# Kernel tuning notes

Measured on AMD Instinct MI355X. Metric: run time of the kernel, lower is better.

The kernel has to match this reference:

```python
import math
import jax, jax.numpy as jnp
import numpy as np

B, A, M, NC = 32, 8400, 32, 80
TOP_K, ALPHA, BETA, EPS = 13, 1.0, 6.0, 1e-9
IMG = 640.0


def _ciou(b1, b2, eps=1e-7):
    # b1, b2 broadcastable [..., 4]; CIoU as in compute_iou (box1=gt, box2=pred)
    b1x1, b1y1, b1x2, b1y2 = b1[..., 0], b1[..., 1], b1[..., 2], b1[..., 3]
    b2x1, b2y1, b2x2, b2y2 = b2[..., 0], b2[..., 1], b2[..., 2], b2[..., 3]
    w1, h1 = b1x2 - b1x1, b1y2 - b1y1 + eps
    w2, h2 = b2x2 - b2x1, b2y2 - b2y1 + eps
    inter = (jnp.minimum(b1x2, b2x2) - jnp.maximum(b1x1, b2x1)).clip(0) * \
            (jnp.minimum(b1y2, b2y2) - jnp.maximum(b1y1, b2y1)).clip(0)
    union = w1 * h1 + w2 * h2 - inter + eps
    iou = inter / union
    cw = jnp.maximum(b1x2, b2x2) - jnp.minimum(b1x1, b2x1)
    ch = jnp.maximum(b1y2, b2y2) - jnp.minimum(b1y1, b2y1)
    c2 = cw ** 2 + ch ** 2 + eps
    rho2 = ((b2x1 + b2x2 - b1x1 - b1x2) ** 2 + (b2y1 + b2y2 - b1y1 - b1y2) ** 2) / 4.0
    v = (4.0 / math.pi ** 2) * (jnp.arctan(w2 / h2) - jnp.arctan(w1 / h1)) ** 2
    alpha = jax.lax.stop_gradient(v / (v - iou + (1.0 + eps)))
    return iou - (rho2 / c2 + v * alpha)


def setup_inputs() -> dict:
    key = jax.random.key(0)
    ks = jax.random.split(key, 8)
    pd_scores = jax.random.uniform(ks[0], (B, A, NC), jnp.float32)
    anc_points = jax.random.uniform(ks[1], (A, 2), jnp.float32) * IMG
    # predicted boxes around anchor points (valid x1<x2, y1<y2)
    off = jax.random.uniform(ks[2], (B, A, 4), jnp.float32) * 80.0 + 2.0
    pd_bboxes = jnp.concatenate([anc_points[None] - off[..., :2],
                                 anc_points[None] + off[..., 2:]], -1)
    # GT boxes: random centers and sizes, clipped to image
    c = jax.random.uniform(ks[3], (B, M, 2), jnp.float32) * IMG
    wh = jax.random.uniform(ks[4], (B, M, 2), jnp.float32) * 180.0 + 20.0
    gt_bboxes = jnp.concatenate([(c - wh / 2).clip(0, IMG), (c + wh / 2).clip(0, IMG)], -1)
    gt_labels = jax.random.randint(ks[5], (B, M, 1), 0, NC, jnp.int64)
    n_valid = jax.random.randint(ks[6], (B,), 1, M + 1)
    mask_gt = (jnp.arange(M)[None, :] < n_valid[:, None]).astype(jnp.float32)[..., None]
    return {"pd_scores": pd_scores, "pd_bboxes": pd_bboxes, "anc_points": anc_points,
            "gt_labels": gt_labels, "gt_bboxes": gt_bboxes, "mask_gt": mask_gt}


def reference(pd_scores, pd_bboxes, anc_points, gt_labels, gt_bboxes, mask_gt):
    b, a, nc = pd_scores.shape
    m = gt_bboxes.shape[1]
    dtype = pd_scores.dtype

    # anchors-inside-GT mask: [B,M,A]
    lt = gt_bboxes[:, :, None, :2]          # [B,M,1,2]
    rb = gt_bboxes[:, :, None, 2:]
    deltas = jnp.concatenate([anc_points[None, None] - lt,
                              rb - anc_points[None, None]], -1)  # [B,M,A,4]
    mask_in_gts = deltas.min(-1) > EPS
    mg = mask_gt[..., 0] > 0                 # [B,M] bool
    gt_mask = mask_in_gts & mg[:, :, None]

    # per-GT class score gather: pd_scores[b, :, gt_labels[b,m]] -> [B,M,A]
    labels = gt_labels[..., 0]               # [B,M]
    idx = jnp.broadcast_to(labels[:, :, None, None], (b, m, a, 1))
    gathered = jnp.take_along_axis(jnp.broadcast_to(pd_scores[:, None], (b, m, a, nc)), idx, axis=3)[..., 0]
    bbox_scores = jnp.where(gt_mask, gathered, 0.0)

    # CIoU overlaps (dense, masked) [B,M,A]
    iou = _ciou(gt_bboxes[:, :, None, :], pd_bboxes[:, None, :, :])
    overlaps = jnp.where(gt_mask, jnp.maximum(iou, 0.0), 0.0)

    align_metric = bbox_scores ** ALPHA * overlaps ** BETA

    # top-k selection with duplicate suppression (faithful to scatter_add loop)
    _, tk_idx = jax.lax.top_k(align_metric, TOP_K)      # [B,M,K]
    tk_mask = jnp.broadcast_to(mg[:, :, None], tk_idx.shape)
    tk_idx = jnp.where(tk_mask, tk_idx, 0)
    bi = jnp.arange(b)[:, None, None]
    mi = jnp.arange(m)[None, :, None]
    counts = jnp.zeros((b, m, a), jnp.int32).at[bi, mi, tk_idx].add(1)
    mask_top_k = jnp.where(counts > 1, 0, counts).astype(dtype)

    mask_pos = mask_top_k * mask_in_gts.astype(dtype) * mg[:, :, None].astype(dtype)
    fg_mask = mask_pos.sum(1)                            # [B,A]

    # resolve anchors assigned to multiple GTs (no-op when none; matches torch branch)
    mask_multi = fg_mask[:, None, :] > 1                 # [B,M,A] (broadcast)
    max_idx = overlaps.argmax(1)                         # [B,A]
    is_max = (jnp.arange(m)[None, :, None] == max_idx[:, None, :]).astype(dtype)
    mask_pos = jnp.where(mask_multi, is_max, mask_pos)
    fg_mask = mask_pos.sum(1)

    target_gt_idx = mask_pos.argmax(1)                   # [B,A]
    target_labels = jnp.maximum(jnp.take_along_axis(labels, target_gt_idx, axis=1), 0)
    target_bboxes = jnp.take_along_axis(
        gt_bboxes, jnp.broadcast_to(target_gt_idx[..., None], (b, a, 4)), axis=1)

    target_scores = jax.nn.one_hot(target_labels, NC, dtype=dtype)
    target_scores = jnp.where((fg_mask > 0)[..., None], target_scores, 0.0)

    am = align_metric * mask_pos
    pos_am = am.max(-1, keepdims=True)                   # [B,M,1]
    pos_ov = (overlaps * mask_pos).max(-1, keepdims=True)
    norm = (am * pos_ov / (pos_am + EPS)).max(1)[..., None]  # [B,A,1]
    target_scores = target_scores * norm

    return target_bboxes, target_scores, fg_mask > 0
```

## Files before the change

### kernel.cpp

```cpp
#include <hip/hip_runtime.h>
#include <math.h>

#define BB 32
#define AA 8400
#define MM 32
#define NCC 80
#define TOPK 13
#define CAP 1024
#define NW (AA / 32 + 1)

__device__ __forceinline__ void wave_argmax(float& v, int& i) {
    #pragma unroll
    for (int off = 32; off > 0; off >>= 1) {
        float ov = __shfl_xor(v, off, 64);
        int oi = __shfl_xor(i, off, 64);
        if (ov > v || (ov == v && oi < i)) { v = ov; i = oi; }
    }
}

__global__ __launch_bounds__(256) void k0_zero(unsigned int* __restrict__ selmask) {
    int g = blockIdx.x * 256 + threadIdx.x;
    if (g < BB * AA / 4) reinterpret_cast<uint4*>(selmask)[g] = uint4{0u, 0u, 0u, 0u};
}

__global__ __launch_bounds__(256) void k12_topk(
        const float* __restrict__ pd_scores, const float* __restrict__ pd_bboxes,
        const float* __restrict__ anc, const int* __restrict__ gt_labels,
        const float* __restrict__ gt_bboxes, const float* __restrict__ mask_gt,
        unsigned int* __restrict__ selmask, float* __restrict__ pos_am, float* __restrict__ pos_ov) {
    __shared__ float lval[CAP];
    __shared__ int   lidx[CAP];
    __shared__ unsigned int bmask[NW];
    __shared__ float wv[4];
    __shared__ int   wi[4];
    __shared__ int   wsum[4];
    __shared__ int   s_p;
    const float eps = 1e-7f;
    int bm = blockIdx.x;
    int b = bm >> 5;
    int m = bm & 31;
    unsigned int mbit = 1u << m;
    int tid = threadIdx.x;
    int lane = tid & 63;
    int wid = tid >> 6;
    if (tid == 0) pos_am[bm] = 0.f;
    if (tid == 1) pos_ov[bm] = 0.f;
    if (!(mask_gt[bm] > 0.f)) return;
    if (tid == 2) s_p = 0;

    for (int i = tid; i < NW; i += 256) bmask[i] = 0u;
    float4 g = reinterpret_cast<const float4*>(gt_bboxes)[bm];

    const float4* anc4 = reinterpret_cast<const float4*>(anc);
    unsigned long long bits = 0ull;
    int c_t = 0;
    #pragma unroll
    for (int j = 0; j < 17; j++) {
        int e = tid + (j << 8);
        if (e < 4200) {
            float4 an = anc4[e];
            float d0 = fminf(fminf(an.x - g.x, an.y - g.y), fminf(g.z - an.x, g.w - an.y));
            float d1 = fminf(fminf(an.z - g.x, an.w - g.y), fminf(g.z - an.z, g.w - an.w));
            if (d0 > 1e-9f) { bits |= 1ull << (2 * j);     c_t++; }
            if (d1 > 1e-9f) { bits |= 1ull << (2 * j + 1); c_t++; }
        }
    }
    int x = c_t;
    #pragma unroll
    for (int off = 1; off < 64; off <<= 1) {
        int y = __shfl_up(x, off, 64);
        if (lane >= off) x += y;
    }
    if (lane == 63) wsum[wid] = x;
    __syncthreads();
    int base = 0;
    #pragma unroll
    for (int w = 0; w < 4; w++) if (w < wid) base += wsum[w];
    int n_c = min(wsum[0] + wsum[1] + wsum[2] + wsum[3], CAP);
    {
        int o = base + x - c_t;
        unsigned long long mm_ = bits;
        while (mm_) {
            int k = __builtin_ctzll(mm_);
            mm_ &= mm_ - 1ull;
            int i = 2 * tid + 512 * (k >> 1) + (k & 1);
            if (o < CAP) lidx[o] = i;
            o++;
        }
    }
    for (int s = n_c + tid; s < CAP; s += 256) { lval[s] = -1.f; lidx[s] = AA; }
    __syncthreads();

    float w1 = g.z - g.x, h1 = g.w - g.y + eps;
    float atg = atanf(w1 / h1);
    float w1h1 = w1 * h1;
    float sgx = g.x + g.z, sgy = g.y + g.w;
    int lab = gt_labels[bm];
    const float4* pbb = reinterpret_cast<const float4*>(pd_bboxes) + (long)b * AA;
    const float* scp = pd_scores + (long)b * AA * NCC + lab;
    int nit = (n_c + 255) >> 8;
    for (int it = 0; it < nit; it++) {
        int s = (it << 8) + tid;
        bool pos = false;
        if (s < n_c) {
            int i = lidx[s];
            float4 pb = pbb[i];
            float w2 = pb.z - pb.x, h2 = pb.w - pb.y + eps;
            float iw = fmaxf(fminf(g.z, pb.z) - fmaxf(g.x, pb.x), 0.f);
            float ih = fmaxf(fminf(g.w, pb.w) - fmaxf(g.y, pb.y), 0.f);
            float inter = iw * ih;
            float uni = w1h1 + w2 * h2 - inter + eps;
            float iou = inter / uni;
            float cw = fmaxf(g.z, pb.z) - fminf(g.x, pb.x);
            float ch = fmaxf(g.w, pb.w) - fminf(g.y, pb.y);
            float c2 = cw * cw + ch * ch + eps;
            float dx = pb.x + pb.z - sgx, dy = pb.y + pb.w - sgy;
            float rho2 = (dx * dx + dy * dy) * 0.25f;
            float dv = atanf(w2 / h2) - atg;
            float v = 0.4052847345693511f * dv * dv;
            float alpha = v / (v - iou + (1.0f + eps));
            float cv = iou - (rho2 / c2 + v * alpha);
            float ov = fmaxf(cv, 0.f);
            float sc = scp[(long)i * NCC];
            float o2 = ov * ov;
            float val = sc * o2 * o2 * o2;
            pos = val > 0.f;
            lval[s] = pos ? val : -1.f;
            if (pos) atomicOr(&bmask[i >> 5], 1u << (i & 31));
        }
        unsigned long long pm = __ballot(pos);
        if (lane == 0) atomicAdd(&s_p, (int)__popcll(pm));
    }
    __syncthreads();
    int p = s_p;

    if (p >= TOPK) {
        float v0 = lval[tid], v1 = lval[tid + 256], v2 = lval[tid + 512], v3 = lval[tid + 768];
        int   i0 = lidx[tid], i1 = lidx[tid + 256], i2 = lidx[tid + 512], i3 = lidx[tid + 768];
        for (int k = 0; k < TOPK; k++) {
            float bv = v0; int bi = i0;
            if (v1 > bv || (v1 == bv && i1 < bi)) { bv = v1; bi = i1; }
            if (v2 > bv || (v2 == bv && i2 < bi)) { bv = v2; bi = i2; }
            if (v3 > bv || (v3 == bv && i3 < bi)) { bv = v3; bi = i3; }
            wave_argmax(bv, bi);
            if (lane == 0) { wv[wid] = bv; wi[wid] = bi; }
            __syncthreads();
            float gv = wv[0]; int gi = wi[0];
            #pragma unroll
            for (int w = 1; w < 4; w++) {
                float ov = wv[w]; int oi = wi[w];
                if (ov > gv || (ov == gv && oi < gi)) { gv = ov; gi = oi; }
            }
            if (tid == 0) atomicOr(&selmask[b * AA + gi], mbit);
            if (i0 == gi) v0 = -1.f;
            if (i1 == gi) v1 = -1.f;
            if (i2 == gi) v2 = -1.f;
            if (i3 == gi) v3 = -1.f;
            __syncthreads();
        }
    } else {
        for (int s = tid; s < n_c; s += 256)
            if (lval[s] > 0.f) atomicOr(&selmask[b * AA + lidx[s]], mbit);
        if (wid == 0) {
            int need = TOPK - p;
            for (int base_i = 0; need > 0 && base_i < AA; base_i += 64) {
                int i = base_i + lane;
                bool cand = (i < AA) && !((bmask[i >> 5] >> (i & 31)) & 1u);
                unsigned long long wm = __ballot(cand);
                int take = min(need, (int)__popcll(wm));
                if (cand && (int)__popcll(wm & ((1ull << lane) - 1ull)) < take) {
                    float2 an = reinterpret_cast<const float2*>(anc)[i];
                    float dmin = fminf(fminf(an.x - g.x, an.y - g.y), fminf(g.z - an.x, g.w - an.y));
                    if (dmin > 1e-9f) atomicOr(&selmask[b * AA + i], mbit);
                }
                need -= take;
            }
        }
    }
}

__global__ __launch_bounds__(256) void k3_resolve(
        const float* __restrict__ pd_scores, const float* __restrict__ pd_bboxes,
        const float* __restrict__ anc, const int* __restrict__ gt_labels,
        const float* __restrict__ gt_bboxes, const float* __restrict__ mask_gt,
        const unsigned int* __restrict__ selmask,
        float* __restrict__ pos_am, float* __restrict__ pos_ov,
        float* __restrict__ out_bbox, float* __restrict__ out_fg,
        float* __restrict__ amval, int* __restrict__ packed) {
    __shared__ float sg[MM][8];
    __shared__ int slab[MM];
    __shared__ int smg[MM];
    const float eps = 1e-7f;
    int b = blockIdx.y;
    int tid = threadIdx.x;
    if (tid < MM) {
        int gm = b * MM + tid;
        float4 g = reinterpret_cast<const float4*>(gt_bboxes)[gm];
        float w1 = g.z - g.x, h1 = g.w - g.y + eps;
        sg[tid][0] = g.x; sg[tid][1] = g.y; sg[tid][2] = g.z; sg[tid][3] = g.w;
        sg[tid][4] = w1 * h1;
        sg[tid][5] = atanf(w1 / h1);
        sg[tid][6] = g.x + g.z;
        sg[tid][7] = g.y + g.w;
        int lb = gt_labels[gm]; if (lb < 0) lb = 0;
        slab[tid] = lb;
        smg[tid] = mask_gt[gm] > 0.f ? 1 : 0;
    }
    __syncthreads();
    int a = blockIdx.x * 256 + tid;
    if (a >= AA) return;
    int g = b * AA + a;
    unsigned int sel = selmask[g];
    int fg = __popc(sel);

    int tg = 0; bool fgo = false; float ovt = 0.f;
    if (fg >= 1) {
        float ax = anc[a * 2], ay = anc[a * 2 + 1];
        float4 pb = reinterpret_cast<const float4*>(pd_bboxes)[g];
        float w2 = pb.z - pb.x, h2 = pb.w - pb.y + eps;
        float atp = atanf(w2 / h2);
        float w2h2 = w2 * h2;
        float spx = pb.x + pb.z, spy = pb.y + pb.w;
        fgo = true;
        if (fg == 1) {
            tg = __ffs(sel) - 1;
            float gx1 = sg[tg][0], gy1 = sg[tg][1], gx2 = sg[tg][2], gy2 = sg[tg][3];
            float iw = fmaxf(fminf(gx2, pb.z) - fmaxf(gx1, pb.x), 0.f);
            float ih = fmaxf(fminf(gy2, pb.w) - fmaxf(gy1, pb.y), 0.f);
            float inter = iw * ih;
            float uni = sg[tg][4] + w2h2 - inter + eps;
            float iou = inter / uni;
            float cw = fmaxf(gx2, pb.z) - fminf(gx1, pb.x);
            float ch = fmaxf(gy2, pb.w) - fminf(gy1, pb.y);
            float c2 = cw * cw + ch * ch + eps;
            float dx = spx - sg[tg][6], dy = spy - sg[tg][7];
            float rho2 = (dx * dx + dy * dy) * 0.25f;
            float dv = atp - sg[tg][5];
            float v = 0.4052847345693511f * dv * dv;
            float alpha = v / (v - iou + (1.0f + eps));
            ovt = fmaxf(iou - (rho2 / c2 + v * alpha), 0.f);
        } else {
            float bestov = -1.f; int bestm = 0;
            for (int mm = 0; mm < MM; mm++) {
                float gx1 = sg[mm][0], gy1 = sg[mm][1], gx2 = sg[mm][2], gy2 = sg[mm][3];
                float dmin = fminf(fminf(ax - gx1, ay - gy1), fminf(gx2 - ax, gy2 - ay));
                float ov = 0.f;
                if ((dmin > 1e-9f) && smg[mm]) {
                    float iw = fmaxf(fminf(gx2, pb.z) - fmaxf(gx1, pb.x), 0.f);
                    float ih = fmaxf(fminf(gy2, pb.w) - fmaxf(gy1, pb.y), 0.f);
                    float inter = iw * ih;
                    float uni = sg[mm][4] + w2h2 - inter + eps;
                    float iou = inter / uni;
                    float cw = fmaxf(gx2, pb.z) - fminf(gx1, pb.x);
                    float ch = fmaxf(gy2, pb.w) - fminf(gy1, pb.y);
                    float c2 = cw * cw + ch * ch + eps;
                    float dx = spx - sg[mm][6], dy = spy - sg[mm][7];
                    float rho2 = (dx * dx + dy * dy) * 0.25f;
                    float dv = atp - sg[mm][5];
                    float v = 0.4052847345693511f * dv * dv;
                    float alpha = v / (v - iou + (1.0f + eps));
                    ov = fmaxf(iou - (rho2 / c2 + v * alpha), 0.f);
                }
                if (ov > bestov) { bestov = ov; bestm = mm; }
            }
            tg = bestm; ovt = bestov;
        }
    }

    float4 gb; gb.x = sg[tg][0]; gb.y = sg[tg][1]; gb.z = sg[tg][2]; gb.w = sg[tg][3];
    reinterpret_cast<float4*>(out_bbox)[g] = gb;
    out_fg[g] = fgo ? 1.f : 0.f;
    float amv = 0.f;
    if (fgo) {
        float sc = pd_scores[(long)g * NCC + slab[tg]];
        float o2 = ovt * ovt;
        amv = sc * o2 * o2 * o2;
        atomicMax((int*)&pos_am[b * MM + tg], __float_as_int(amv));
        atomicMax((int*)&pos_ov[b * MM + tg], __float_as_int(ovt));
    }
    amval[g] = amv;
    packed[g] = tg | (slab[tg] << 8) | ((fgo ? 1 : 0) << 16);
}

__global__ __launch_bounds__(256) void k4_scores(
        const float* __restrict__ amval, const int* __restrict__ packed,
        const float* __restrict__ pos_am, const float* __restrict__ pos_ov,
        float* __restrict__ out_scores) {
    int g = blockIdx.x * 256 + threadIdx.x;
    const int NQ = NCC / 4;
    if (g >= BB * AA * NQ) return;
    int ba = g / NQ;
    int c0 = (g % NQ) * 4;
    float4 o = {0.f, 0.f, 0.f, 0.f};
    int p = packed[ba];
    if (p & (1 << 16)) {
        int tg = p & 31, lab = (p >> 8) & 127;
        int b = ba / AA;
        int bm = b * MM + tg;
        float nv = (amval[ba] * pos_ov[bm]) / (pos_am[bm] + 1e-9f);
        int d = lab - c0;
        if (d == 0) o.x = nv; else if (d == 1) o.y = nv;
        else if (d == 2) o.z = nv; else if (d == 3) o.w = nv;
    }
    reinterpret_cast<float4*>(out_scores)[g] = o;
}

extern "C" void kernel_launch(void* const* d_in, const int* in_sizes, int n_in,
                              void* d_out, int out_size, void* d_ws, size_t ws_size,
                              hipStream_t stream) {
    const float* pd_scores = (const float*)d_in[0];
    const float* pd_bboxes = (const float*)d_in[1];
    const float* anc       = (const float*)d_in[2];
    const int*   gt_labels = (const int*)d_in[3];
    const float* gt_bboxes = (const float*)d_in[4];
    const float* mask_gt   = (const float*)d_in[5];

    const long nBA = (long)BB * AA;

    char* ws = (char*)d_ws;
    unsigned int* selmask = (unsigned int*)ws;  ws += nBA * 4;
    float* pos_am = (float*)ws;                 ws += BB * MM * 4;
    float* pos_ov = (float*)ws;                 ws += BB * MM * 4;
    float* amval  = (float*)ws;                 ws += nBA * 4;
    int*   packed = (int*)ws;                   ws += nBA * 4;

    float* out_bbox   = (float*)d_out;
    float* out_scores = out_bbox + nBA * 4;
    float* out_fg     = out_scores + nBA * NCC;

    k0_zero<<<(int)((nBA / 4 + 255) / 256), 256, 0, stream>>>(selmask);
    k12_topk<<<BB * MM, 256, 0, stream>>>(pd_scores, pd_bboxes, anc, gt_labels,
                                          gt_bboxes, mask_gt, selmask, pos_am, pos_ov);
    dim3 g3((AA + 255) / 256, BB);
    k3_resolve<<<g3, 256, 0, stream>>>(pd_scores, pd_bboxes, anc, gt_labels,
                                       gt_bboxes, mask_gt, selmask, pos_am, pos_ov,
                                       out_bbox, out_fg, amval, packed);
    long nS4 = nBA * (NCC / 4);
    k4_scores<<<(int)((nS4 + 255) / 256), 256, 0, stream>>>(amval, packed, pos_am, pos_ov, out_scores);
}
```

Baseline: 190.5 us.

## Widen top-k blocks, remap block order, pack metadata, use nontemporal stores

The top-k kernel now runs 512 threads per block. Each thread preloads its anchor float4s up front, and block indices are remapped so neighbouring blocks cover different images. The score load is hoisted ahead of the CIoU math, and the 13 selection atomics are deferred to one batch after the loop. The resolve and scores kernels exchange a single packed int2 per anchor instead of two separate arrays, and the large output writes use nontemporal stores to bypass cache. The aim is to cut latency in the per-GT top-k pass and reduce memory traffic in the output-bound kernels. The cost is more register pressure and block-wide syncs across 8 waves.

Measured after the change: 195.0 us. 2.4% more time.

```diff
diff --git a/kernel.cpp b/kernel.cpp
--- a/kernel.cpp
+++ b/kernel.cpp
@@ -8,6 +8,9 @@
 #define TOPK 13
 #define CAP 1024
 #define NW (AA / 32 + 1)
+#define K12T 512
+
+typedef float nfloat4 __attribute__((ext_vector_type(4)));
 
 __device__ __forceinline__ void wave_argmax(float& v, int& i) {
     #pragma unroll
@@ -23,7 +26,7 @@
     if (g < BB * AA / 4) reinterpret_cast<uint4*>(selmask)[g] = uint4{0u, 0u, 0u, 0u};
 }
 
-__global__ __launch_bounds__(256) void k12_topk(
+__global__ __launch_bounds__(K12T) void k12_topk(
         const float* __restrict__ pd_scores, const float* __restrict__ pd_bboxes,
         const float* __restrict__ anc, const int* __restrict__ gt_labels,
         const float* __restrict__ gt_bboxes, const float* __restrict__ mask_gt,
@@ -31,39 +34,44 @@
     __shared__ float lval[CAP];
     __shared__ int   lidx[CAP];
     __shared__ unsigned int bmask[NW];
-    __shared__ float wv[4];
-    __shared__ int   wi[4];
-    __shared__ int   wsum[4];
+    __shared__ float wv[8];
+    __shared__ int   wi[8];
+    __shared__ int   wsum[8];
     __shared__ int   s_p;
     const float eps = 1e-7f;
-    int bm = blockIdx.x;
-    int b = bm >> 5;
-    int m = bm & 31;
+    int ib = blockIdx.x;
+    int b = (ib & 7) + ((ib >> 8) << 3);
+    int m = (ib >> 3) & 31;
+    int bm = b * MM + m;
     unsigned int mbit = 1u << m;
     int tid = threadIdx.x;
     int lane = tid & 63;
     int wid = tid >> 6;
     if (tid == 0) pos_am[bm] = 0.f;
     if (tid == 1) pos_ov[bm] = 0.f;
+    if (tid == 2) s_p = 0;
     if (!(mask_gt[bm] > 0.f)) return;
-    if (tid == 2) s_p = 0;
-
-    for (int i = tid; i < NW; i += 256) bmask[i] = 0u;
+
+    for (int i = tid; i < NW; i += K12T) bmask[i] = 0u;
     float4 g = reinterpret_cast<const float4*>(gt_bboxes)[bm];
 
     const float4* anc4 = reinterpret_cast<const float4*>(anc);
-    unsigned long long bits = 0ull;
+    float4 av[9];
+    #pragma unroll
+    for (int j = 0; j < 9; j++) {
+        int e = tid + (j << 9);
+        av[j] = anc4[e > 4199 ? 4199 : e];
+    }
+    unsigned int bits = 0u;
     int c_t = 0;
     #pragma unroll
-    for (int j = 0; j < 17; j++) {
-        int e = tid + (j << 8);
-        if (e < 4200) {
-            float4 an = anc4[e];
-            float d0 = fminf(fminf(an.x - g.x, an.y - g.y), fminf(g.z - an.x, g.w - an.y));
-            float d1 = fminf(fminf(an.z - g.x, an.w - g.y), fminf(g.z - an.z, g.w - an.w));
-            if (d0 > 1e-9f) { bits |= 1ull << (2 * j);     c_t++; }
-            if (d1 > 1e-9f) { bits |= 1ull << (2 * j + 1); c_t++; }
-        }
+    for (int j = 0; j < 9; j++) {
+        int e = tid + (j << 9);
+        bool valid = e < 4200;
+        float d0 = fminf(fminf(av[j].x - g.x, av[j].y - g.y), fminf(g.z - av[j].x, g.w - av[j].y));
+        float d1 = fminf(fminf(av[j].z - g.x, av[j].w - g.y), fminf(g.z - av[j].z, g.w - av[j].w));
+        if (valid && d0 > 1e-9f) { bits |= 1u << (2 * j);     c_t++; }
+        if (valid && d1 > 1e-9f) { bits |= 1u << (2 * j + 1); c_t++; }
     }
     int x = c_t;
     #pragma unroll
@@ -73,22 +81,22 @@
     }
     if (lane == 63) wsum[wid] = x;
     __syncthreads();
-    int base = 0;
-    #pragma unroll
-    for (int w = 0; w < 4; w++) if (w < wid) base += wsum[w];
-    int n_c = min(wsum[0] + wsum[1] + wsum[2] + wsum[3], CAP);
+    int base = 0, tot = 0;
+    #pragma unroll
+    for (int w = 0; w < 8; w++) { if (w < wid) base += wsum[w]; tot += wsum[w]; }
+    int n_c = min(tot, CAP);
     {
         int o = base + x - c_t;
-        unsigned long long mm_ = bits;
+        unsigned int mm_ = bits;
         while (mm_) {
-            int k = __builtin_ctzll(mm_);
-            mm_ &= mm_ - 1ull;
-            int i = 2 * tid + 512 * (k >> 1) + (k & 1);
+            int k = __builtin_ctz(mm_);
+            mm_ &= mm_ - 1u;
+            int i = 2 * tid + ((k >> 1) << 10) + (k & 1);
             if (o < CAP) lidx[o] = i;
             o++;
         }
     }
-    for (int s = n_c + tid; s < CAP; s += 256) { lval[s] = -1.f; lidx[s] = AA; }
+    for (int s = n_c + tid; s < CAP; s += K12T) { lval[s] = -1.f; lidx[s] = AA; }
     __syncthreads();
 
     float w1 = g.z - g.x, h1 = g.w - g.y + eps;
@@ -98,13 +106,14 @@
     int lab = gt_labels[bm];
     const float4* pbb = reinterpret_cast<const float4*>(pd_bboxes) + (long)b * AA;
     const float* scp = pd_scores + (long)b * AA * NCC + lab;
-    int nit = (n_c + 255) >> 8;
+    int nit = (n_c + K12T - 1) >> 9;
     for (int it = 0; it < nit; it++) {
-        int s = (it << 8) + tid;
+        int s = (it << 9) + tid;
         bool pos = false;
         if (s < n_c) {
             int i = lidx[s];
             float4 pb = pbb[i];
+            float sc = scp[(long)i * NCC];
             float w2 = pb.z - pb.x, h2 = pb.w - pb.y + eps;
             float iw = fmaxf(fminf(g.z, pb.z) - fmaxf(g.x, pb.x), 0.f);
             float ih = fmaxf(fminf(g.w, pb.w) - fmaxf(g.y, pb.y), 0.f);
@@ -121,7 +130,6 @@
             float alpha = v / (v - iou + (1.0f + eps));
             float cv = iou - (rho2 / c2 + v * alpha);
             float ov = fmaxf(cv, 0.f);
-            float sc = scp[(long)i * NCC];
             float o2 = ov * ov;
             float val = sc * o2 * o2 * o2;
             pos = val > 0.f;
@@ -135,31 +143,29 @@
     int p = s_p;
 
     if (p >= TOPK) {
-        float v0 = lval[tid], v1 = lval[tid + 256], v2 = lval[tid + 512], v3 = lval[tid + 768];
-        int   i0 = lidx[tid], i1 = lidx[tid + 256], i2 = lidx[tid + 512], i3 = lidx[tid + 768];
+        float v0 = lval[tid], v1 = lval[tid + 512];
+        int   i0 = lidx[tid], i1 = lidx[tid + 512];
+        int mysel = -1;
         for (int k = 0; k < TOPK; k++) {
             float bv = v0; int bi = i0;
             if (v1 > bv || (v1 == bv && i1 < bi)) { bv = v1; bi = i1; }
-            if (v2 > bv || (v2 == bv && i2 < bi)) { bv = v2; bi = i2; }
-            if (v3 > bv || (v3 == bv && i3 < bi)) { bv = v3; bi = i3; }
             wave_argmax(bv, bi);
             if (lane == 0) { wv[wid] = bv; wi[wid] = bi; }
             __syncthreads();
             float gv = wv[0]; int gi = wi[0];
             #pragma unroll
-            for (int w = 1; w < 4; w++) {
+            for (int w = 1; w < 8; w++) {
                 float ov = wv[w]; int oi = wi[w];
                 if (ov > gv || (ov == gv && oi < gi)) { gv = ov; gi = oi; }
             }
-            if (tid == 0) atomicOr(&selmask[b * AA + gi], mbit);
+            if (tid == k) mysel = gi;
             if (i0 == gi) v0 = -1.f;
             if (i1 == gi) v1 = -1.f;
-            if (i2 == gi) v2 = -1.f;
-            if (i3 == gi) v3 = -1.f;
             __syncthreads();
         }
+        if (tid < TOPK) atomicOr(&selmask[b * AA + mysel], mbit);
     } else {
-        for (int s = tid; s < n_c; s += 256)
+        for (int s = tid; s < n_c; s += K12T)
             if (lval[s] > 0.f) atomicOr(&selmask[b * AA + lidx[s]], mbit);
         if (wid == 0) {
             int need = TOPK - p;
@@ -186,7 +192,7 @@
         const unsigned int* __restrict__ selmask,
         float* __restrict__ pos_am, float* __restrict__ pos_ov,
         float* __restrict__ out_bbox, float* __restrict__ out_fg,
-        float* __restrict__ amval, int* __restrict__ packed) {
+        int2* __restrict__ meta) {
     __shared__ float sg[MM][8];
     __shared__ int slab[MM];
     __shared__ int smg[MM];
@@ -267,8 +273,8 @@
         }
     }
 
-    float4 gb; gb.x = sg[tg][0]; gb.y = sg[tg][1]; gb.z = sg[tg][2]; gb.w = sg[tg][3];
-    reinterpret_cast<float4*>(out_bbox)[g] = gb;
+    nfloat4 gb = {sg[tg][0], sg[tg][1], sg[tg][2], sg[tg][3]};
+    __builtin_nontemporal_store(gb, reinterpret_cast<nfloat4*>(out_bbox) + g);
     out_fg[g] = fgo ? 1.f : 0.f;
     float amv = 0.f;
     if (fgo) {
@@ -278,12 +284,11 @@
         atomicMax((int*)&pos_am[b * MM + tg], __float_as_int(amv));
         atomicMax((int*)&pos_ov[b * MM + tg], __float_as_int(ovt));
     }
-    amval[g] = amv;
-    packed[g] = tg | (slab[tg] << 8) | ((fgo ? 1 : 0) << 16);
+    meta[g] = make_int2(__float_as_int(amv), tg | (slab[tg] << 8) | ((fgo ? 1 : 0) << 16));
 }
 
 __global__ __launch_bounds__(256) void k4_scores(
-        const float* __restrict__ amval, const int* __restrict__ packed,
+        const int2* __restrict__ meta,
         const float* __restrict__ pos_am, const float* __restrict__ pos_ov,
         float* __restrict__ out_scores) {
     int g = blockIdx.x * 256 + threadIdx.x;
@@ -291,18 +296,19 @@
     if (g >= BB * AA * NQ) return;
     int ba = g / NQ;
     int c0 = (g % NQ) * 4;
-    float4 o = {0.f, 0.f, 0.f, 0.f};
-    int p = packed[ba];
+    nfloat4 o = {0.f, 0.f, 0.f, 0.f};
+    int2 mt = meta[ba];
+    int p = mt.y;
     if (p & (1 << 16)) {
         int tg = p & 31, lab = (p >> 8) & 127;
         int b = ba / AA;
         int bm = b * MM + tg;
-        float nv = (amval[ba] * pos_ov[bm]) / (pos_am[bm] + 1e-9f);
+        float nv = (__int_as_float(mt.x) * pos_ov[bm]) / (pos_am[bm] + 1e-9f);
         int d = lab - c0;
         if (d == 0) o.x = nv; else if (d == 1) o.y = nv;
         else if (d == 2) o.z = nv; else if (d == 3) o.w = nv;
     }
-    reinterpret_cast<float4*>(out_scores)[g] = o;
+    __builtin_nontemporal_store(o, reinterpret_cast<nfloat4*>(out_scores) + g);
 }
 
 extern "C" void kernel_launch(void* const* d_in, const int* in_sizes, int n_in,
@@ -321,20 +327,19 @@
     unsigned int* selmask = (unsigned int*)ws;  ws += nBA * 4;
     float* pos_am = (float*)ws;                 ws += BB * MM * 4;
     float* pos_ov = (float*)ws;                 ws += BB * MM * 4;
-    float* amval  = (float*)ws;                 ws += nBA * 4;
-    int*   packed = (int*)ws;                   ws += nBA * 4;
+    int2*  meta   = (int2*)ws;                  ws += nBA * 8;
 
     float* out_bbox   = (float*)d_out;
     float* out_scores = out_bbox + nBA * 4;
     float* out_fg     = out_scores + nBA * NCC;
 
     k0_zero<<<(int)((nBA / 4 + 255) / 256), 256, 0, stream>>>(selmask);
-    k12_topk<<<BB * MM, 256, 0, stream>>>(pd_scores, pd_bboxes, anc, gt_labels,
-                                          gt_bboxes, mask_gt, selmask, pos_am, pos_ov);
+    k12_topk<<<BB * MM, K12T, 0, stream>>>(pd_scores, pd_bboxes, anc, gt_labels,
+                                           gt_bboxes, mask_gt, selmask, pos_am, pos_ov);
     dim3 g3((AA + 255) / 256, BB);
     k3_resolve<<<g3, 256, 0, stream>>>(pd_scores, pd_bboxes, anc, gt_labels,
                                        gt_bboxes, mask_gt, selmask, pos_am, pos_ov,
-                                       out_bbox, out_fg, amval, packed);
+                                       out_bbox, out_fg, meta);
     long nS4 = nBA * (NCC / 4);
-    k4_scores<<<(int)((nS4 + 255) / 256), 256, 0, stream>>>(amval, packed, pos_am, pos_ov, out_scores);
-}
+    k4_scores<<<(int)((nS4 + 255) / 256), 256, 0, stream>>>(meta, pos_am, pos_ov, out_scores);
+}
```
